# Kernel optimization log

Measured on AMD Instinct MI355X. Metric: run time of the kernel, lower is better.

## Reference

```python
import jax, jax.numpy as jnp
import numpy as np

N_BITS = 16
V = 1 << N_BITS  # 65536 possible 16-bit patterns


def setup_inputs() -> dict:
    key = jax.random.key(0)
    k1, k2, k3 = jax.random.split(key, 3)
    B, H, T = 16, 128, 4096
    W = jax.random.normal(k1, (B, H, N_BITS), dtype=jnp.float32) * 0.5  # per-bit weights
    r = jax.random.normal(k2, (B, H), dtype=jnp.float32)                 # per-hidden phase/bias
    # x holds raw 16-bit patterns (indices into the 2^16 support)
    x = jax.random.randint(k3, (B, T), 0, V, dtype=jnp.int32)
    return {"x": x, "W": W, "r": r}


def _logits_all(W, r):
    """Logit of every one of the 2^16 representable values. [B, V]"""
    enum = jnp.arange(V, dtype=jnp.int32)
    shifts = jnp.arange(N_BITS, dtype=jnp.int32)
    bits = ((enum[:, None] >> shifts[None, :]) & 1).astype(W.dtype)  # [V, N]
    z = jnp.einsum('vn,bhn->bvh', bits, W) + r[:, None, :]           # [B, V, H]
    return jnp.cos(z).sum(axis=-1)                                    # [B, V]


def reference(x, W, r):
    """BIDE forward: log_prob(x) = logit(bits(x)) - logsumexp over all 2^N patterns."""
    logits = _logits_all(W, r)                       # [B, V]
    logZ = jax.nn.logsumexp(logits, axis=1)          # [B]  exact partition over full support
    logit_x = jnp.take_along_axis(logits, x, axis=1) # [B, T] gather by bit-pattern index
    return logit_x - logZ[:, None]
```

## Files before the change

### kernel.cpp

```cpp
#include <hip/hip_runtime.h>
#include <hip/hip_bf16.h>

#define BDIM 16
#define HDIM 128
#define TDIM 4096
#define VSZ  65536

typedef __attribute__((ext_vector_type(8))) short bf16x8;
typedef __attribute__((ext_vector_type(4))) float f32x4;

static __device__ __forceinline__ unsigned int f2bf(float f) {
  unsigned int u = __float_as_uint(f);
  return (u + 0x7fffu + ((u >> 16) & 1u)) >> 16;
}

__global__ __launch_bounds__(512) void bide_logits_mfma(
    const float* __restrict__ W, const float* __restrict__ r,
    float* __restrict__ logits, float* __restrict__ partM,
    float* __restrict__ partS) {
  __shared__ unsigned int stg[2][64 * 32];
  __shared__ float red[16];

  int bid = blockIdx.x;
  int b    = bid >> 4;
  int tile = bid & 15;
  int tlo = (tile & 3) * 64;
  int thi = (tile >> 2) * 64;
  int tid = threadIdx.x;

  int tab  = tid >> 8;
  int srow = tid & 63;
  int grp  = (tid >> 6) & 3;
  int sval = (tab ? tlo : thi) + srow;
  int woff = tab ? 0 : 8;

  int l = tid & 63;
  int w = tid >> 6;
  int rowblk = w & 3, colhalf = w >> 2;
  int r15 = l & 15, kl = l >> 4;
  int arow  = rowblk * 16 + r15;
  int brow0 = colhalf * 32 + r15;
  int brow1 = brow0 + 16;

  const float* Wb = W + b * HDIM * 16;
  const float* rb = r + b * HDIM;

  f32x4 acc0 = {0.f, 0.f, 0.f, 0.f};
  f32x4 acc1 = {0.f, 0.f, 0.f, 0.f};

  const bf16x8* U8 = (const bf16x8*)stg[0];
  const bf16x8* V8 = (const bf16x8*)stg[1];
  unsigned int* stow = stg[tab];

  for (int kc = 0; kc < 4; ++kc) {
    int hbase = kc * 32;
    __syncthreads();
#pragma unroll
    for (int e = 0; e < 8; ++e) {
      int hp = grp * 8 + e;
      int h = hbase + hp;
      const float* Wp = Wb + h * 16 + woff;
      float sacc = tab ? rb[h] : 0.f;
#pragma unroll
      for (int n = 0; n < 8; ++n)
        sacc = fmaf((float)((sval >> n) & 1), Wp[n], sacc);
      float sn, cs;
      __sincosf(sacc, &sn, &cs);
      if (!tab) sn = -sn;
      stow[srow * 32 + (hp ^ ((srow & 7) << 2))] = f2bf(cs) | (f2bf(sn) << 16);
    }
    __syncthreads();

#pragma unroll
    for (int ks = 0; ks < 2; ++ks) {
      bf16x8 a  = U8[arow  * 8 + ((ks * 4 + kl) ^ (arow  & 7))];
      bf16x8 b0 = V8[brow0 * 8 + ((ks * 4 + kl) ^ (brow0 & 7))];
      bf16x8 b1 = V8[brow1 * 8 + ((ks * 4 + kl) ^ (brow1 & 7))];
      acc0 = __builtin_amdgcn_mfma_f32_16x16x32_bf16(a, b0, acc0, 0, 0, 0);
      acc1 = __builtin_amdgcn_mfma_f32_16x16x32_bf16(a, b1, acc1, 0, 0, 0);
    }
  }

  float* Lb = logits + b * VSZ;
  int orow = thi + rowblk * 16 + 4 * kl;
  int ocol = tlo + colhalf * 32 + r15;
#pragma unroll
  for (int q = 0; q < 4; ++q) {
    Lb[(orow + q) * 256 + ocol]      = acc0[q];
    Lb[(orow + q) * 256 + ocol + 16] = acc1[q];
  }

  float m = fmaxf(fmaxf(fmaxf(acc0[0], acc0[1]), fmaxf(acc0[2], acc0[3])),
                  fmaxf(fmaxf(acc1[0], acc1[1]), fmaxf(acc1[2], acc1[3])));
#pragma unroll
  for (int off = 1; off < 64; off <<= 1) m = fmaxf(m, __shfl_xor(m, off, 64));
  if (l == 0) red[w] = m;
  __syncthreads();
  float M = red[0];
#pragma unroll
  for (int i = 1; i < 8; ++i) M = fmaxf(M, red[i]);
  float s = 0.f;
#pragma unroll
  for (int q = 0; q < 4; ++q)
    s += __expf(acc0[q] - M) + __expf(acc1[q] - M);
#pragma unroll
  for (int off = 1; off < 64; off <<= 1) s += __shfl_xor(s, off, 64);
  if (l == 0) red[8 + w] = s;
  __syncthreads();
  if (tid == 0) {
    float S = 0.f;
#pragma unroll
    for (int i = 0; i < 8; ++i) S += red[8 + i];
    partM[bid] = M;
    partS[bid] = S;
  }
}

__global__ __launch_bounds__(256) void bide_out(
    const float* __restrict__ logits,
    const float* __restrict__ partM, const float* __restrict__ partS,
    const int* __restrict__ x, float* __restrict__ out) {
  int bid = blockIdx.x;
  int b   = bid >> 4;
  int seg = bid & 15;
  int tid = threadIdx.x;
  __shared__ float s_logZ;
  if (tid < 64) {
    float m  = (tid < 16) ? partM[b * 16 + tid] : -1e30f;
    float sv = (tid < 16) ? partS[b * 16 + tid] : 0.f;
    float M = m;
#pragma unroll
    for (int off = 1; off < 16; off <<= 1) M = fmaxf(M, __shfl_xor(M, off, 16));
    float z = sv * __expf(m - M);
#pragma unroll
    for (int off = 1; off < 16; off <<= 1) z += __shfl_xor(z, off, 16);
    if (tid == 0) s_logZ = M + __logf(z);
  }
  __syncthreads();
  int t = seg * 256 + tid;
  int vidx = x[b * TDIM + t];
  out[b * TDIM + t] = logits[b * VSZ + vidx] - s_logZ;
}

extern "C" void kernel_launch(void* const* d_in, const int* in_sizes, int n_in,
                              void* d_out, int out_size, void* d_ws, size_t ws_size,
                              hipStream_t stream) {
  const int*   x = (const int*)d_in[0];
  const float* W = (const float*)d_in[1];
  const float* r = (const float*)d_in[2];
  float* out = (float*)d_out;

  float* logits = (float*)d_ws;
  float* partM  = logits + BDIM * VSZ;
  float* partS  = partM + 256;

  bide_logits_mfma<<<BDIM * 16, 512, 0, stream>>>(W, r, logits, partM, partS);
  bide_out<<<BDIM * TDIM / 256, 256, 0, stream>>>(logits, partM, partS, x, out);
}
```

Before: 70.85 us.

## Fuse logit gather into main kernel via LDS tile, drop global logits buffer

Each block no longer writes its 64x64 logits tile to a 4 MB global workspace. It stages the tile transposed and swizzled in LDS, then scans all 4096 x values for its batch and writes out only the entries whose index falls in its tile. A small second kernel merges the per-tile max and sum into logZ and subtracts it in place using float4 accesses. The staging loop also writes two packed bf16 pairs per store and hoists the bit-to-float conversion. The cost is that every block reads the full x row for its batch, plus extra LDS and branchy scattered output writes.

```diff
diff --git a/kernel.cpp b/kernel.cpp
--- a/kernel.cpp
+++ b/kernel.cpp
@@ -14,11 +14,12 @@
   return (u + 0x7fffu + ((u >> 16) & 1u)) >> 16;
 }
 
-__global__ __launch_bounds__(512) void bide_logits_mfma(
+__global__ __launch_bounds__(512) void bide_main(
     const float* __restrict__ W, const float* __restrict__ r,
-    float* __restrict__ logits, float* __restrict__ partM,
-    float* __restrict__ partS) {
+    const int* __restrict__ x, float* __restrict__ out,
+    float* __restrict__ partM, float* __restrict__ partS) {
   __shared__ unsigned int stg[2][64 * 32];
+  __shared__ float ldsT[64 * 64];
   __shared__ float red[16];
 
   int bid = blockIdx.x;
@@ -33,6 +34,7 @@
   int grp  = (tid >> 6) & 3;
   int sval = (tab ? tlo : thi) + srow;
   int woff = tab ? 0 : 8;
+  int swz  = (srow & 7) << 2;
 
   int l = tid & 63;
   int w = tid >> 6;
@@ -45,6 +47,10 @@
   const float* Wb = W + b * HDIM * 16;
   const float* rb = r + b * HDIM;
 
+  float fb[8];
+#pragma unroll
+  for (int n = 0; n < 8; ++n) fb[n] = (float)((sval >> n) & 1);
+
   f32x4 acc0 = {0.f, 0.f, 0.f, 0.f};
   f32x4 acc1 = {0.f, 0.f, 0.f, 0.f};
 
@@ -56,18 +62,24 @@
     int hbase = kc * 32;
     __syncthreads();
 #pragma unroll
-    for (int e = 0; e < 8; ++e) {
+    for (int e = 0; e < 8; e += 2) {
       int hp = grp * 8 + e;
-      int h = hbase + hp;
-      const float* Wp = Wb + h * 16 + woff;
-      float sacc = tab ? rb[h] : 0.f;
+      unsigned int uu0, uu1;
 #pragma unroll
-      for (int n = 0; n < 8; ++n)
-        sacc = fmaf((float)((sval >> n) & 1), Wp[n], sacc);
-      float sn, cs;
-      __sincosf(sacc, &sn, &cs);
-      if (!tab) sn = -sn;
-      stow[srow * 32 + (hp ^ ((srow & 7) << 2))] = f2bf(cs) | (f2bf(sn) << 16);
+      for (int p = 0; p < 2; ++p) {
+        int h = hbase + hp + p;
+        const float* Wp = Wb + h * 16 + woff;
+        float sacc = tab ? rb[h] : 0.f;
+#pragma unroll
+        for (int n = 0; n < 8; ++n) sacc = fmaf(fb[n], Wp[n], sacc);
+        float sn, cs;
+        __sincosf(sacc, &sn, &cs);
+        if (!tab) sn = -sn;
+        unsigned int uv = f2bf(cs) | (f2bf(sn) << 16);
+        if (p == 0) uu0 = uv; else uu1 = uv;
+      }
+      int idx = srow * 32 + (hp ^ swz);
+      *(uint2*)&stow[idx] = make_uint2(uu0, uu1);
     }
     __syncthreads();
 
@@ -81,13 +93,12 @@
     }
   }
 
-  float* Lb = logits + b * VSZ;
-  int orow = thi + rowblk * 16 + 4 * kl;
-  int ocol = tlo + colhalf * 32 + r15;
-#pragma unroll
-  for (int q = 0; q < 4; ++q) {
-    Lb[(orow + q) * 256 + ocol]      = acc0[q];
-    Lb[(orow + q) * 256 + ocol + 16] = acc1[q];
+  {
+    int c0  = colhalf * 32 + r15;
+    int rb0 = rowblk * 16 + 4 * kl;
+    int sw  = (c0 & 7) << 3;
+    *(f32x4*)&ldsT[c0 * 64 + (rb0 ^ sw)]        = acc0;
+    *(f32x4*)&ldsT[(c0 + 16) * 64 + (rb0 ^ sw)] = acc1;
   }
 
   float m = fmaxf(fmaxf(fmaxf(acc0[0], acc0[1]), fmaxf(acc0[2], acc0[3])),
@@ -114,32 +125,43 @@
     partM[bid] = M;
     partS[bid] = S;
   }
+
+  const int4* x4 = (const int4*)(x + b * TDIM);
+  float* ob = out + b * TDIM;
+#pragma unroll
+  for (int it = 0; it < 2; ++it) {
+    int4 xv = x4[tid + it * 512];
+    int tbase = 4 * (tid + it * 512);
+    int vv[4] = {xv.x, xv.y, xv.z, xv.w};
+#pragma unroll
+    for (int j = 0; j < 4; ++j) {
+      int v = vv[j];
+      int tl = ((v >> 14) << 2) | ((v >> 6) & 3);
+      if (tl == tile) {
+        int row = (v >> 8) & 63, col = v & 63;
+        ob[tbase + j] = ldsT[col * 64 + (row ^ ((col & 7) << 3))];
+      }
+    }
+  }
 }
 
-__global__ __launch_bounds__(256) void bide_out(
-    const float* __restrict__ logits,
-    const float* __restrict__ partM, const float* __restrict__ partS,
-    const int* __restrict__ x, float* __restrict__ out) {
+__global__ __launch_bounds__(256) void bide_sub(
+    float* __restrict__ out, const float* __restrict__ partM,
+    const float* __restrict__ partS) {
   int bid = blockIdx.x;
-  int b   = bid >> 4;
-  int seg = bid & 15;
-  int tid = threadIdx.x;
-  __shared__ float s_logZ;
-  if (tid < 64) {
-    float m  = (tid < 16) ? partM[b * 16 + tid] : -1e30f;
-    float sv = (tid < 16) ? partS[b * 16 + tid] : 0.f;
-    float M = m;
+  int b = bid >> 2, seg = bid & 3;
+  float M = -1e30f;
 #pragma unroll
-    for (int off = 1; off < 16; off <<= 1) M = fmaxf(M, __shfl_xor(M, off, 16));
-    float z = sv * __expf(m - M);
+  for (int i = 0; i < 16; ++i) M = fmaxf(M, partM[b * 16 + i]);
+  float S = 0.f;
 #pragma unroll
-    for (int off = 1; off < 16; off <<= 1) z += __shfl_xor(z, off, 16);
-    if (tid == 0) s_logZ = M + __logf(z);
-  }
-  __syncthreads();
-  int t = seg * 256 + tid;
-  int vidx = x[b * TDIM + t];
-  out[b * TDIM + t] = logits[b * VSZ + vidx] - s_logZ;
+  for (int i = 0; i < 16; ++i)
+    S += partS[b * 16 + i] * __expf(partM[b * 16 + i] - M);
+  float logZ = M + __logf(S);
+  float4* o4 = (float4*)(out + b * TDIM + seg * 1024);
+  float4 v = o4[threadIdx.x];
+  v.x -= logZ; v.y -= logZ; v.z -= logZ; v.w -= logZ;
+  o4[threadIdx.x] = v;
 }
 
 extern "C" void kernel_launch(void* const* d_in, const int* in_sizes, int n_in,
@@ -150,10 +172,9 @@
   const float* r = (const float*)d_in[2];
   float* out = (float*)d_out;
 
-  float* logits = (float*)d_ws;
-  float* partM  = logits + BDIM * VSZ;
-  float* partS  = partM + 256;
+  float* partM = (float*)d_ws;
+  float* partS = partM + 256;
 
-  bide_logits_mfma<<<BDIM * 16, 512, 0, stream>>>(W, r, logits, partM, partS);
-  bide_out<<<BDIM * TDIM / 256, 256, 0, stream>>>(logits, partM, partS, x, out);
+  bide_main<<<BDIM * 16, 512, 0, stream>>>(W, r, x, out, partM, partS);
+  bide_sub<<<64, 256, 0, stream>>>(out, partM, partS);
 }
```

Result: faster. 69.16 us (median of 2 runs) (-2.4%).
